# Performance work log

Hardware: AMD Instinct MI355X
Metric: run time of the kernel (lower is better)

## Reference

```python
import jax, jax.numpy as jnp
import numpy as np

B, S, DIM = 2, 2048, 2048
N_HEADS, N_KV_HEADS = 16, 4
HEAD_DIM = DIM // N_HEADS  # 128
N_REP = N_HEADS // N_KV_HEADS  # 4


def setup_inputs() -> dict:
    key = jax.random.key(0)
    ks = jax.random.split(key, 7)
    x = jax.random.normal(ks[0], (B, S, DIM), dtype=jnp.float32)
    cos = jax.random.uniform(ks[1], (S, HEAD_DIM // 2), dtype=jnp.float32)
    sin = jax.random.uniform(ks[2], (S, HEAD_DIM // 2), dtype=jnp.float32)
    sc = 1.0 / np.sqrt(DIM)
    wq = jax.random.normal(ks[3], (DIM, N_HEADS * HEAD_DIM), dtype=jnp.float32) * sc
    wk = jax.random.normal(ks[4], (DIM, N_KV_HEADS * HEAD_DIM), dtype=jnp.float32) * sc
    wv = jax.random.normal(ks[5], (DIM, N_KV_HEADS * HEAD_DIM), dtype=jnp.float32) * sc
    wo = jax.random.normal(ks[6], (N_HEADS * HEAD_DIM, DIM), dtype=jnp.float32) * sc
    return {"x": x, "cos": cos, "sin": sin, "wq": wq, "wk": wk, "wv": wv, "wo": wo}


def _rope(t, cos, sin):
    # t: [B, S, H, hd]; cos/sin: [S, hd/2] -> broadcast as [1, S, 1, hd/2]
    tr, ti = t[..., ::2], t[..., 1::2]
    c = cos[None, :, None, :]
    s = sin[None, :, None, :]
    out_r = tr * c - ti * s
    out_i = tr * s + ti * c
    # interleave back: stack on new last axis then flatten
    return jnp.stack([out_r, out_i], axis=-1).reshape(t.shape)


def reference(x, cos, sin, wq, wk, wv, wo):
    bsz, seqlen, _ = x.shape
    xq = (x @ wq).reshape(bsz, seqlen, N_HEADS, HEAD_DIM)
    xk = (x @ wk).reshape(bsz, seqlen, N_KV_HEADS, HEAD_DIM)
    xv = (x @ wv).reshape(bsz, seqlen, N_KV_HEADS, HEAD_DIM)
    xq = _rope(xq, cos, sin)
    xk = _rope(xk, cos, sin)
    # GQA: repeat kv heads -> [B, S, H, hd]
    xk = jnp.repeat(xk, N_REP, axis=2)
    xv = jnp.repeat(xv, N_REP, axis=2)
    scale = 1.0 / jnp.sqrt(jnp.asarray(HEAD_DIM, dtype=x.dtype))
    scores = jnp.einsum("bqhd,bkhd->bhqk", xq, xk) * scale
    causal = jnp.tril(jnp.ones((seqlen, seqlen), dtype=bool))
    scores = jnp.where(causal[None, None, :, :], scores, jnp.asarray(-jnp.inf, dtype=scores.dtype))
    attn = jax.nn.softmax(scores, axis=-1)
    out = jnp.einsum("bhqk,bkhd->bqhd", attn, xv)
    out = out.reshape(bsz, seqlen, N_HEADS * HEAD_DIM)
    return out @ wo
```

## Files before the change

kernel.cpp:

```cpp
#include <hip/hip_runtime.h>
#include <stdint.h>

#define SEQ 2048

typedef uint16_t u16;
typedef uint32_t u32;
typedef __attribute__((ext_vector_type(4))) float f32x4;
typedef __attribute__((ext_vector_type(8))) __bf16 bf16x8;

__device__ __forceinline__ u16 f2bf(float f) {
    u32 u = __float_as_uint(f);
    u += 0x7FFFu + ((u >> 16) & 1u);
    return (u16)(u >> 16);
}
__device__ __forceinline__ float bf2f(u16 h) {
    return __uint_as_float(((u32)h) << 16);
}
__device__ __forceinline__ void async16(const void* g, void* l) {
    auto gp = (__attribute__((address_space(1))) void*)const_cast<void*>(g);
    auto lp = (__attribute__((address_space(3))) void*)l;
    __builtin_amdgcn_global_load_lds(gp, lp, 16, 0, 0);
}

__global__ __launch_bounds__(256) void convert_bf16(const float* __restrict__ src,
                                                    u16* __restrict__ dst) {
    int i = blockIdx.x * 256 + threadIdx.x;
    float4 v = ((const float4*)src)[i];
    u32 lo = (u32)f2bf(v.x) | ((u32)f2bf(v.y) << 16);
    u32 hi = (u32)f2bf(v.z) | ((u32)f2bf(v.w) << 16);
    ((uint2*)dst)[i] = make_uint2(lo, hi);
}

__global__ __launch_bounds__(256) void tconv(const float* __restrict__ src,
                                             u16* __restrict__ dst, int N, int K) {
    __shared__ float tile[64][65];
    const int n0 = blockIdx.x * 64, k0 = blockIdx.y * 64;
    const int tid = threadIdx.x;
#pragma unroll
    for (int p = 0; p < 4; p++) {
        int r = p * 16 + (tid >> 4);
        int c = (tid & 15) * 4;
        float4 v = *(const float4*)&src[(size_t)(k0 + r) * N + n0 + c];
        tile[r][c] = v.x; tile[r][c+1] = v.y; tile[r][c+2] = v.z; tile[r][c+3] = v.w;
    }
    __syncthreads();
#pragma unroll
    for (int p = 0; p < 4; p++) {
        int n = p * 16 + (tid >> 4);
        int kq = (tid & 15) * 4;
        u32 lo = (u32)f2bf(tile[kq+0][n]) | ((u32)f2bf(tile[kq+1][n]) << 16);
        u32 hi = (u32)f2bf(tile[kq+2][n]) | ((u32)f2bf(tile[kq+3][n]) << 16);
        *(uint2*)&dst[(size_t)(n0 + n) * K + k0 + kq] = make_uint2(lo, hi);
    }
}

template <bool F32OUT>
__global__ __launch_bounds__(256) void gemm128(const u16* __restrict__ A,
                                               const u16* __restrict__ Bt,
                                               void* __restrict__ Cv,
                                               int M, int N, int K) {
    __shared__ u16 lA[128 * 32];
    __shared__ u16 lB[128 * 32];
    const int tid = threadIdx.x;
    const int m0 = blockIdx.y * 128, n0 = blockIdx.x * 128;
    const int lane = tid & 63;
    const int lr = lane & 15, quad = lane >> 4;
    const int w = tid >> 6;
    const int wm = (w >> 1) * 64, wn = (w & 1) * 64;

    f32x4 acc[4][4] = {};

    const int srow = tid >> 2;
    const int schunk = (tid & 3) ^ (srow & 3);
    const u16* aS0 = A  + (size_t)(m0 + srow) * K + schunk * 8;
    const u16* aS1 = aS0 + (size_t)64 * K;
    const u16* bS0 = Bt + (size_t)(n0 + srow) * K + schunk * 8;
    const u16* bS1 = bS0 + (size_t)64 * K;
    u16* lAd = lA + tid * 8;
    u16* lBd = lB + tid * 8;

    for (int k0 = 0; k0 < K; k0 += 32) {
        __syncthreads();
        async16(aS0 + k0, lAd);
        async16(aS1 + k0, lAd + 2048);
        async16(bS0 + k0, lBd);
        async16(bS1 + k0, lBd + 2048);
        __syncthreads();
        bf16x8 af[4], bfr[4];
        const int cs = (quad ^ (lr & 3)) * 8;
#pragma unroll
        for (int i = 0; i < 4; i++)
            af[i] = *(const bf16x8*)&lA[(wm + i * 16 + lr) * 32 + cs];
#pragma unroll
        for (int i = 0; i < 4; i++)
            bfr[i] = *(const bf16x8*)&lB[(wn + i * 16 + lr) * 32 + cs];
#pragma unroll
        for (int mf = 0; mf < 4; mf++)
#pragma unroll
            for (int nf = 0; nf < 4; nf++)
                acc[mf][nf] = __builtin_amdgcn_mfma_f32_16x16x32_bf16(
                    af[mf], bfr[nf], acc[mf][nf], 0, 0, 0);
    }

#pragma unroll
    for (int mf = 0; mf < 4; mf++) {
#pragma unroll
        for (int nf = 0; nf < 4; nf++) {
#pragma unroll
            for (int r = 0; r < 4; r++) {
                size_t row = (size_t)(m0 + wm + mf * 16 + quad * 4 + r);
                size_t col = (size_t)(n0 + wn + nf * 16 + lr);
                if (F32OUT)
                    ((float*)Cv)[row * (size_t)N + col] = acc[mf][nf][r];
                else
                    ((u16*)Cv)[row * (size_t)N + col] = f2bf(acc[mf][nf][r]);
            }
        }
    }
}

__global__ __launch_bounds__(256) void rope_qk(u16* __restrict__ qkv,
                                               const float* __restrict__ cosp,
                                               const float* __restrict__ sinp) {
    const int t = blockIdx.x;
    const int spos = t & (SEQ - 1);
    const int tid = threadIdx.x;
    const float qscale = 0.088388347762f * 1.4426950408889634f;
    u16* row = qkv + (size_t)t * 3072;
#pragma unroll
    for (int it = 0; it < 5; it++) {
        int p = it * 256 + tid;
        int col, ci; float sc2;
        if (p < 1024) { col = 2 * p; ci = p & 63; sc2 = qscale; }
        else          { int p2 = p - 1024; col = 2048 + 2 * p2; ci = p2 & 63; sc2 = 1.0f; }
        u32 v = *(u32*)(row + col);
        float tr = bf2f((u16)(v & 0xFFFFu));
        float ti = bf2f((u16)(v >> 16));
        float cs = cosp[spos * 64 + ci];
        float sn = sinp[spos * 64 + ci];
        float orr = (tr * cs - ti * sn) * sc2;
        float oi  = (tr * sn + ti * cs) * sc2;
        *(u32*)(row + col) = (u32)f2bf(orr) | ((u32)f2bf(oi) << 16);
    }
}

__global__ __launch_bounds__(256) void transpose_v(const u16* __restrict__ qkv,
                                                   u16* __restrict__ vt) {
    __shared__ u16 tile[64][65];
    const int bid = blockIdx.x;
    const int dt = bid & 1;
    const int st = (bid >> 1) & 31;
    const int kh = (bid >> 6) & 3;
    const int b  = bid >> 8;
    const int tid = threadIdx.x;
#pragma unroll
    for (int pp = 0; pp < 2; pp++) {
        int r  = pp * 32 + (tid >> 3);
        int c8 = (tid & 7) * 8;
        const u16* src = qkv + (size_t)(b * SEQ + st * 64 + r) * 3072 + 2560 + kh * 128 + dt * 64 + c8;
        uint4 v = *(const uint4*)src;
        tile[r][c8+0] = (u16)(v.x & 0xFFFF); tile[r][c8+1] = (u16)(v.x >> 16);
        tile[r][c8+2] = (u16)(v.y & 0xFFFF); tile[r][c8+3] = (u16)(v.y >> 16);
        tile[r][c8+4] = (u16)(v.z & 0xFFFF); tile[r][c8+5] = (u16)(v.z >> 16);
        tile[r][c8+6] = (u16)(v.w & 0xFFFF); tile[r][c8+7] = (u16)(v.w >> 16);
    }
    __syncthreads();
#pragma unroll
    for (int pp = 0; pp < 2; pp++) {
        int dr = pp * 32 + (tid >> 3);
        int s8 = (tid & 7) * 8;
        uint4 o;
        o.x = (u32)tile[s8+0][dr] | ((u32)tile[s8+1][dr] << 16);
        o.y = (u32)tile[s8+2][dr] | ((u32)tile[s8+3][dr] << 16);
        o.z = (u32)tile[s8+4][dr] | ((u32)tile[s8+5][dr] << 16);
        o.w = (u32)tile[s8+6][dr] | ((u32)tile[s8+7][dr] << 16);
        u16* dst = vt + ((size_t)((b * 4 + kh) * 128 + dt * 64 + dr)) * SEQ + st * 64 + s8;
        *(uint4*)dst = o;
    }
}

__global__ __launch_bounds__(256) void flash_attn(const u16* __restrict__ qkv,
                                                  const u16* __restrict__ vt,
                                                  u16* __restrict__ ob) {
    __shared__ u16 lK[2][64 * 128];
    __shared__ u16 lV[2][128 * 64];
    __shared__ u16 lP[4 * 16 * 64];
    const int bidx = blockIdx.x;
    const int qa = bidx & 15;
    const int h  = (bidx >> 4) & 15;
    const int b  = bidx >> 8;
    const int kh = h >> 2;
    const int tid = threadIdx.x;
    const int w = tid >> 6, lane = tid & 63;
    const int lr = lane & 15, quad = lane >> 4;

    const int krow = tid >> 4;
    const int kchunk = (tid & 15) ^ krow;
    const int vrow = tid >> 3;
    const int vchunk = (tid & 7) ^ (vrow & 7);
    const u16* kRow = qkv + (size_t)b * SEQ * 3072 + 2048 + kh * 128
                    + (size_t)krow * 3072 + kchunk * 8;
    const u16* vRow = vt + (size_t)(b * 4 + kh) * 128 * SEQ
                    + (size_t)vrow * SEQ + vchunk * 8;

    for (int half = 0; half < 2; half++) {
        const int qt = half ? qa : (31 - qa);

        bf16x8 qf[4];
        {
            const u16* qbase = qkv + (size_t)(b * SEQ + qt * 64 + w * 16 + lr) * 3072 + h * 128;
#pragma unroll
            for (int kk = 0; kk < 4; kk++)
                qf[kk] = *(const bf16x8*)(qbase + kk * 32 + quad * 8);
        }

        f32x4 o[8] = {};
        float mrow[4] = {-1e30f, -1e30f, -1e30f, -1e30f};
        float lrow[4] = {0.f, 0.f, 0.f, 0.f};

        {
            u16* lKd = &lK[0][0] + tid * 8;
            u16* lVd = &lV[0][0] + tid * 8;
#pragma unroll
            for (int i = 0; i < 4; i++)
                async16(kRow + (size_t)(i * 16) * 3072, lKd + i * 2048);
#pragma unroll
            for (int i = 0; i < 4; i++)
                async16(vRow + (size_t)(i * 32) * SEQ, lVd + i * 2048);
        }

        int nb = 0;
        for (int kt = 0; kt <= qt; kt++) {
            if (kt < qt) {
                u16* lKd = &lK[nb ^ 1][0] + tid * 8;
                u16* lVd = &lV[nb ^ 1][0] + tid * 8;
#pragma unroll
                for (int i = 0; i < 4; i++)
                    async16(kRow + (size_t)((kt + 1) * 64 + i * 16) * 3072, lKd + i * 2048);
#pragma unroll
                for (int i = 0; i < 4; i++)
                    async16(vRow + (size_t)(i * 32) * SEQ + (kt + 1) * 64, lVd + i * 2048);
                asm volatile("s_waitcnt vmcnt(8)" ::: "memory");
            } else {
                asm volatile("s_waitcnt vmcnt(0)" ::: "memory");
            }
            asm volatile("s_barrier" ::: "memory");

            const u16* lKc = &lK[nb][0];
            const u16* lVc = &lV[nb][0];

            f32x4 sc[4] = {};
#pragma unroll
            for (int nf = 0; nf < 4; nf++) {
#pragma unroll
                for (int kk = 0; kk < 4; kk++) {
                    bf16x8 bk = *(const bf16x8*)&lKc[(nf * 16 + lr) * 128 + (((kk * 4 + quad) ^ lr) * 8)];
                    sc[nf] = __builtin_amdgcn_mfma_f32_16x16x32_bf16(qf[kk], bk, sc[nf], 0, 0, 0);
                }
            }

            float sv[4][4];
            float mnew[4] = {mrow[0], mrow[1], mrow[2], mrow[3]};
            const bool diag = (kt == qt);
#pragma unroll
            for (int nf = 0; nf < 4; nf++)
#pragma unroll
                for (int r = 0; r < 4; r++) {
                    float v = sc[nf][r];
                    if (diag && (nf * 16 + lr) > (w * 16 + quad * 4 + r)) v = -1e30f;
                    sv[nf][r] = v;
                    mnew[r] = fmaxf(mnew[r], v);
                }
#pragma unroll
            for (int r = 0; r < 4; r++) {
                mnew[r] = fmaxf(mnew[r], __shfl_xor(mnew[r], 1, 16));
                mnew[r] = fmaxf(mnew[r], __shfl_xor(mnew[r], 2, 16));
                mnew[r] = fmaxf(mnew[r], __shfl_xor(mnew[r], 4, 16));
                mnew[r] = fmaxf(mnew[r], __shfl_xor(mnew[r], 8, 16));
            }
            float rsum[4] = {0.f, 0.f, 0.f, 0.f};
#pragma unroll
            for (int nf = 0; nf < 4; nf++)
#pragma unroll
                for (int r = 0; r < 4; r++) {
                    float e = exp2f(sv[nf][r] - mnew[r]);
                    sv[nf][r] = e;
                    rsum[r] += e;
                }
#pragma unroll
            for (int r = 0; r < 4; r++) {
                rsum[r] += __shfl_xor(rsum[r], 1, 16);
                rsum[r] += __shfl_xor(rsum[r], 2, 16);
                rsum[r] += __shfl_xor(rsum[r], 4, 16);
                rsum[r] += __shfl_xor(rsum[r], 8, 16);
            }
#pragma unroll
            for (int r = 0; r < 4; r++) {
                float alpha = exp2f(mrow[r] - mnew[r]);
                lrow[r] = lrow[r] * alpha + rsum[r];
                mrow[r] = mnew[r];
#pragma unroll
                for (int f = 0; f < 8; f++) o[f][r] *= alpha;
            }

#pragma unroll
            for (int nf = 0; nf < 4; nf++)
#pragma unroll
                for (int r = 0; r < 4; r++) {
                    int m_ = quad * 4 + r;
                    int khi = nf * 2 + (lr >> 3);
                    lP[w * 1024 + m_ * 64 + ((khi ^ (m_ & 7)) * 8) + (lr & 7)] = f2bf(sv[nf][r]);
                }

#pragma unroll
            for (int kf = 0; kf < 2; kf++) {
                bf16x8 pa = *(const bf16x8*)&lP[w * 1024 + lr * 64 + (((kf * 4 + quad) ^ (lr & 7)) * 8)];
#pragma unroll
                for (int nf = 0; nf < 8; nf++) {
                    bf16x8 vb = *(const bf16x8*)&lVc[(nf * 16 + lr) * 64 + (((kf * 4 + quad) ^ (lr & 7)) * 8)];
                    o[nf] = __builtin_amdgcn_mfma_f32_16x16x32_bf16(pa, vb, o[nf], 0, 0, 0);
                }
            }

            asm volatile("s_barrier" ::: "memory");
            nb ^= 1;
        }

        u16* obase = ob + (size_t)(b * SEQ + qt * 64 + w * 16) * 2048 + h * 128;
#pragma unroll
        for (int r = 0; r < 4; r++) {
            float rinv = 1.0f / lrow[r];
#pragma unroll
            for (int f = 0; f < 8; f++)
                obase[(quad * 4 + r) * 2048 + f * 16 + lr] = f2bf(o[f][r] * rinv);
        }
    }
}

extern "C" void kernel_launch(void* const* d_in, const int* in_sizes, int n_in,
                              void* d_out, int out_size, void* d_ws, size_t ws_size,
                              hipStream_t stream) {
    (void)in_sizes; (void)n_in; (void)out_size; (void)ws_size;
    const float* x    = (const float*)d_in[0];
    const float* cosp = (const float*)d_in[1];
    const float* sinp = (const float*)d_in[2];
    const float* wq   = (const float*)d_in[3];
    const float* wk   = (const float*)d_in[4];
    const float* wv   = (const float*)d_in[5];
    const float* wo   = (const float*)d_in[6];
    float* out = (float*)d_out;

    char* ws = (char*)d_ws;
    u16* xb    = (u16*)(ws);
    u16* qkvb  = (u16*)(ws + (size_t)16 * 1024 * 1024);
    u16* wqkvT = (u16*)(ws + (size_t)40 * 1024 * 1024);
    u16* woT   = (u16*)(ws + (size_t)52 * 1024 * 1024);
    u16* vtb   = (u16*)(ws + (size_t)60 * 1024 * 1024);
    u16* ob    = xb;

    convert_bf16<<<8192, 256, 0, stream>>>(x, xb);
    tconv<<<dim3(32, 32), 256, 0, stream>>>(wq, wqkvT, 2048, 2048);
    tconv<<<dim3( 8, 32), 256, 0, stream>>>(wk, wqkvT + (size_t)2048 * 2048, 512, 2048);
    tconv<<<dim3( 8, 32), 256, 0, stream>>>(wv, wqkvT + (size_t)2560 * 2048, 512, 2048);
    tconv<<<dim3(32, 32), 256, 0, stream>>>(wo, woT, 2048, 2048);
    gemm128<false><<<dim3(24, 32), 256, 0, stream>>>(xb, wqkvT, (void*)qkvb, 4096, 3072, 2048);
    rope_qk<<<4096, 256, 0, stream>>>(qkvb, cosp, sinp);
    transpose_v<<<512, 256, 0, stream>>>(qkvb, vtb);
    flash_attn<<<512, 256, 0, stream>>>(qkvb, vtb, ob);
    gemm128<true><<<dim3(16, 32), 256, 0, stream>>>(ob, woT, (void*)out, 4096, 2048, 2048);
}
```

Measured before the change: 363.0 us.

## Use 128-row query tiles with transposed S=K·Q^T MFMA and per-lane row softmax

The flash attention kernel now gives each block a 128-query tile, with each wave holding 32 query rows, so every K/V tile loaded into LDS feeds twice as many MFMAs. It replaces the paired-half scheme with a heavy-first block ordering. Scores are computed as K·Q^T, so each lane owns one query row, which reduces the softmax reductions to two cross-quad shuffles. P is written to LDS as packed 4-element stores. The cost is higher register pressure from doubled accumulators under launch_bounds(256,2), plus fewer, larger blocks with coarser load balance.

```diff
diff --git a/kernel.cpp b/kernel.cpp
--- a/kernel.cpp
+++ b/kernel.cpp
@@ -7,6 +7,7 @@
 typedef uint32_t u32;
 typedef __attribute__((ext_vector_type(4))) float f32x4;
 typedef __attribute__((ext_vector_type(8))) __bf16 bf16x8;
+typedef __attribute__((ext_vector_type(4))) __bf16 bf16x4;
 
 __device__ __forceinline__ u16 f2bf(float f) {
     u32 u = __float_as_uint(f);
@@ -179,20 +180,29 @@
     }
 }
 
-__global__ __launch_bounds__(256) void flash_attn(const u16* __restrict__ qkv,
-                                                  const u16* __restrict__ vt,
-                                                  u16* __restrict__ ob) {
+__global__ __launch_bounds__(256, 2) void flash_attn(const u16* __restrict__ qkv,
+                                                     const u16* __restrict__ vt,
+                                                     u16* __restrict__ ob) {
     __shared__ u16 lK[2][64 * 128];
     __shared__ u16 lV[2][128 * 64];
-    __shared__ u16 lP[4 * 16 * 64];
+    __shared__ u16 lP[4][32 * 64];
     const int bidx = blockIdx.x;
-    const int qa = bidx & 15;
-    const int h  = (bidx >> 4) & 15;
-    const int b  = bidx >> 8;
-    const int kh = h >> 2;
+    int bh, qt;
+    if (bidx < 256) { bh = bidx >> 3;         qt = 8 + (bidx & 7); }
+    else            { bh = (bidx - 256) >> 3; qt = 7 - ((bidx - 256) & 7); }
+    const int b = bh >> 4, h = bh & 15, kh = h >> 2;
     const int tid = threadIdx.x;
     const int w = tid >> 6, lane = tid & 63;
     const int lr = lane & 15, quad = lane >> 4;
+
+    bf16x8 qf[2][4];
+#pragma unroll
+    for (int qi = 0; qi < 2; qi++) {
+        const u16* qbase = qkv + (size_t)(b * SEQ + qt * 128 + w * 32 + qi * 16 + lr) * 3072 + h * 128;
+#pragma unroll
+        for (int kk = 0; kk < 4; kk++)
+            qf[qi][kk] = *(const bf16x8*)(qbase + kk * 32 + quad * 8);
+    }
 
     const int krow = tid >> 4;
     const int kchunk = (tid & 15) ^ krow;
@@ -203,136 +213,133 @@
     const u16* vRow = vt + (size_t)(b * 4 + kh) * 128 * SEQ
                     + (size_t)vrow * SEQ + vchunk * 8;
 
-    for (int half = 0; half < 2; half++) {
-        const int qt = half ? qa : (31 - qa);
-
-        bf16x8 qf[4];
-        {
-            const u16* qbase = qkv + (size_t)(b * SEQ + qt * 64 + w * 16 + lr) * 3072 + h * 128;
-#pragma unroll
-            for (int kk = 0; kk < 4; kk++)
-                qf[kk] = *(const bf16x8*)(qbase + kk * 32 + quad * 8);
-        }
-
-        f32x4 o[8] = {};
-        float mrow[4] = {-1e30f, -1e30f, -1e30f, -1e30f};
-        float lrow[4] = {0.f, 0.f, 0.f, 0.f};
-
-        {
-            u16* lKd = &lK[0][0] + tid * 8;
-            u16* lVd = &lV[0][0] + tid * 8;
+    f32x4 o[2][8] = {};
+    float m_st[2] = {-1e30f, -1e30f};
+    float l_st[2] = {0.f, 0.f};
+
+    const int nkt = 2 * qt + 2;
+    {
+        u16* lKd = &lK[0][0] + tid * 8;
+        u16* lVd = &lV[0][0] + tid * 8;
+#pragma unroll
+        for (int i = 0; i < 4; i++) async16(kRow + (size_t)(i * 16) * 3072, lKd + i * 2048);
+#pragma unroll
+        for (int i = 0; i < 4; i++) async16(vRow + (size_t)(i * 32) * SEQ, lVd + i * 2048);
+    }
+    const int qg = qt * 128 + w * 32 + lr;
+
+    int nb = 0;
+    for (int kt = 0; kt < nkt; kt++) {
+        if (kt + 1 < nkt) {
+            u16* lKd = &lK[nb ^ 1][0] + tid * 8;
+            u16* lVd = &lV[nb ^ 1][0] + tid * 8;
 #pragma unroll
             for (int i = 0; i < 4; i++)
-                async16(kRow + (size_t)(i * 16) * 3072, lKd + i * 2048);
+                async16(kRow + (size_t)((kt + 1) * 64 + i * 16) * 3072, lKd + i * 2048);
 #pragma unroll
             for (int i = 0; i < 4; i++)
-                async16(vRow + (size_t)(i * 32) * SEQ, lVd + i * 2048);
-        }
-
-        int nb = 0;
-        for (int kt = 0; kt <= qt; kt++) {
-            if (kt < qt) {
-                u16* lKd = &lK[nb ^ 1][0] + tid * 8;
-                u16* lVd = &lV[nb ^ 1][0] + tid * 8;
-#pragma unroll
-                for (int i = 0; i < 4; i++)
-                    async16(kRow + (size_t)((kt + 1) * 64 + i * 16) * 3072, lKd + i * 2048);
-#pragma unroll
-                for (int i = 0; i < 4; i++)
-                    async16(vRow + (size_t)(i * 32) * SEQ + (kt + 1) * 64, lVd + i * 2048);
-                asm volatile("s_waitcnt vmcnt(8)" ::: "memory");
-            } else {
-                asm volatile("s_waitcnt vmcnt(0)" ::: "memory");
-            }
-            asm volatile("s_barrier" ::: "memory");
-
-            const u16* lKc = &lK[nb][0];
-            const u16* lVc = &lV[nb][0];
-
-            f32x4 sc[4] = {};
+                async16(vRow + (size_t)(i * 32) * SEQ + (kt + 1) * 64, lVd + i * 2048);
+            asm volatile("s_waitcnt vmcnt(8)" ::: "memory");
+        } else {
+            asm volatile("s_waitcnt vmcnt(0)" ::: "memory");
+        }
+        asm volatile("s_barrier" ::: "memory");
+
+        const u16* lKc = &lK[nb][0];
+        const u16* lVc = &lV[nb][0];
+
+        f32x4 sc[2][4] = {};
+#pragma unroll
+        for (int nf = 0; nf < 4; nf++) {
+#pragma unroll
+            for (int kk = 0; kk < 4; kk++) {
+                bf16x8 ak = *(const bf16x8*)&lKc[(nf * 16 + lr) * 128 + (((kk * 4 + quad) ^ lr) * 8)];
+                sc[0][nf] = __builtin_amdgcn_mfma_f32_16x16x32_bf16(ak, qf[0][kk], sc[0][nf], 0, 0, 0);
+                sc[1][nf] = __builtin_amdgcn_mfma_f32_16x16x32_bf16(ak, qf[1][kk], sc[1][nf], 0, 0, 0);
+            }
+        }
+
+        const bool diag = (kt >= 2 * qt);
+        const int kb = kt * 64 + quad * 4;
+#pragma unroll
+        for (int qi = 0; qi < 2; qi++) {
+            float ps[4][4];
+            float mnew = m_st[qi];
+            const int qrow_g = qg + qi * 16;
+#pragma unroll
+            for (int nf = 0; nf < 4; nf++)
+#pragma unroll
+                for (int r = 0; r < 4; r++) {
+                    float v = sc[qi][nf][r];
+                    if (diag && (kb + nf * 16 + r) > qrow_g) v = -1e30f;
+                    ps[nf][r] = v;
+                    mnew = fmaxf(mnew, v);
+                }
+            mnew = fmaxf(mnew, __shfl_xor(mnew, 16));
+            mnew = fmaxf(mnew, __shfl_xor(mnew, 32));
+            float rsum = 0.f;
+#pragma unroll
+            for (int nf = 0; nf < 4; nf++)
+#pragma unroll
+                for (int r = 0; r < 4; r++) {
+                    float e = exp2f(ps[nf][r] - mnew);
+                    ps[nf][r] = e;
+                    rsum += e;
+                }
+            rsum += __shfl_xor(rsum, 16);
+            rsum += __shfl_xor(rsum, 32);
+            float alpha = exp2f(m_st[qi] - mnew);
+            l_st[qi] = l_st[qi] * alpha + rsum;
+            m_st[qi] = mnew;
+#pragma unroll
+            for (int r = 0; r < 4; r++) {
+                float ar = __shfl(alpha, quad * 4 + r, 16);
+#pragma unroll
+                for (int nd = 0; nd < 8; nd++) o[qi][nd][r] *= ar;
+            }
+            const int qrow = qi * 16 + lr;
 #pragma unroll
             for (int nf = 0; nf < 4; nf++) {
-#pragma unroll
-                for (int kk = 0; kk < 4; kk++) {
-                    bf16x8 bk = *(const bf16x8*)&lKc[(nf * 16 + lr) * 128 + (((kk * 4 + quad) ^ lr) * 8)];
-                    sc[nf] = __builtin_amdgcn_mfma_f32_16x16x32_bf16(qf[kk], bk, sc[nf], 0, 0, 0);
-                }
-            }
-
-            float sv[4][4];
-            float mnew[4] = {mrow[0], mrow[1], mrow[2], mrow[3]};
-            const bool diag = (kt == qt);
-#pragma unroll
-            for (int nf = 0; nf < 4; nf++)
-#pragma unroll
-                for (int r = 0; r < 4; r++) {
-                    float v = sc[nf][r];
-                    if (diag && (nf * 16 + lr) > (w * 16 + quad * 4 + r)) v = -1e30f;
-                    sv[nf][r] = v;
-                    mnew[r] = fmaxf(mnew[r], v);
-                }
-#pragma unroll
-            for (int r = 0; r < 4; r++) {
-                mnew[r] = fmaxf(mnew[r], __shfl_xor(mnew[r], 1, 16));
-                mnew[r] = fmaxf(mnew[r], __shfl_xor(mnew[r], 2, 16));
-                mnew[r] = fmaxf(mnew[r], __shfl_xor(mnew[r], 4, 16));
-                mnew[r] = fmaxf(mnew[r], __shfl_xor(mnew[r], 8, 16));
-            }
-            float rsum[4] = {0.f, 0.f, 0.f, 0.f};
-#pragma unroll
-            for (int nf = 0; nf < 4; nf++)
-#pragma unroll
-                for (int r = 0; r < 4; r++) {
-                    float e = exp2f(sv[nf][r] - mnew[r]);
-                    sv[nf][r] = e;
-                    rsum[r] += e;
-                }
-#pragma unroll
-            for (int r = 0; r < 4; r++) {
-                rsum[r] += __shfl_xor(rsum[r], 1, 16);
-                rsum[r] += __shfl_xor(rsum[r], 2, 16);
-                rsum[r] += __shfl_xor(rsum[r], 4, 16);
-                rsum[r] += __shfl_xor(rsum[r], 8, 16);
-            }
-#pragma unroll
-            for (int r = 0; r < 4; r++) {
-                float alpha = exp2f(mrow[r] - mnew[r]);
-                lrow[r] = lrow[r] * alpha + rsum[r];
-                mrow[r] = mnew[r];
-#pragma unroll
-                for (int f = 0; f < 8; f++) o[f][r] *= alpha;
-            }
-
-#pragma unroll
-            for (int nf = 0; nf < 4; nf++)
-#pragma unroll
-                for (int r = 0; r < 4; r++) {
-                    int m_ = quad * 4 + r;
-                    int khi = nf * 2 + (lr >> 3);
-                    lP[w * 1024 + m_ * 64 + ((khi ^ (m_ & 7)) * 8) + (lr & 7)] = f2bf(sv[nf][r]);
-                }
-
-#pragma unroll
-            for (int kf = 0; kf < 2; kf++) {
-                bf16x8 pa = *(const bf16x8*)&lP[w * 1024 + lr * 64 + (((kf * 4 + quad) ^ (lr & 7)) * 8)];
-#pragma unroll
-                for (int nf = 0; nf < 8; nf++) {
-                    bf16x8 vb = *(const bf16x8*)&lVc[(nf * 16 + lr) * 64 + (((kf * 4 + quad) ^ (lr & 7)) * 8)];
-                    o[nf] = __builtin_amdgcn_mfma_f32_16x16x32_bf16(pa, vb, o[nf], 0, 0, 0);
-                }
-            }
-
-            asm volatile("s_barrier" ::: "memory");
-            nb ^= 1;
-        }
-
-        u16* obase = ob + (size_t)(b * SEQ + qt * 64 + w * 16) * 2048 + h * 128;
+                u32 lo = (u32)f2bf(ps[nf][0]) | ((u32)f2bf(ps[nf][1]) << 16);
+                u32 hi = (u32)f2bf(ps[nf][2]) | ((u32)f2bf(ps[nf][3]) << 16);
+                int c = (nf * 4 + quad) ^ lr;
+                *(uint2*)&lP[w][qrow * 64 + c * 4] = make_uint2(lo, hi);
+            }
+        }
+
+#pragma unroll
+        for (int kf = 0; kf < 2; kf++) {
+            bf16x8 pa[2];
+#pragma unroll
+            for (int qi = 0; qi < 2; qi++) {
+                int c0 = (kf * 8 + quad * 2) ^ lr;
+                int c1 = (kf * 8 + quad * 2 + 1) ^ lr;
+                bf16x4 p0 = *(const bf16x4*)&lP[w][(qi * 16 + lr) * 64 + c0 * 4];
+                bf16x4 p1 = *(const bf16x4*)&lP[w][(qi * 16 + lr) * 64 + c1 * 4];
+                pa[qi] = __builtin_shufflevector(p0, p1, 0, 1, 2, 3, 4, 5, 6, 7);
+            }
+#pragma unroll
+            for (int nd = 0; nd < 8; nd++) {
+                bf16x8 vb = *(const bf16x8*)&lVc[(nd * 16 + lr) * 64 + (((kf * 4 + quad) ^ (lr & 7)) * 8)];
+                o[0][nd] = __builtin_amdgcn_mfma_f32_16x16x32_bf16(pa[0], vb, o[0][nd], 0, 0, 0);
+                o[1][nd] = __builtin_amdgcn_mfma_f32_16x16x32_bf16(pa[1], vb, o[1][nd], 0, 0, 0);
+            }
+        }
+
+        asm volatile("s_barrier" ::: "memory");
+        nb ^= 1;
+    }
+
+#pragma unroll
+    for (int qi = 0; qi < 2; qi++) {
+        float rinv = 1.0f / l_st[qi];
+        u16* obase = ob + (size_t)(b * SEQ + qt * 128 + w * 32 + qi * 16) * 2048 + h * 128;
 #pragma unroll
         for (int r = 0; r < 4; r++) {
-            float rinv = 1.0f / lrow[r];
-#pragma unroll
-            for (int f = 0; f < 8; f++)
-                obase[(quad * 4 + r) * 2048 + f * 16 + lr] = f2bf(o[f][r] * rinv);
+            float rv = __shfl(rinv, quad * 4 + r, 16);
+#pragma unroll
+            for (int nd = 0; nd < 8; nd++)
+                obase[(quad * 4 + r) * 2048 + nd * 16 + lr] = f2bf(o[qi][nd][r] * rv);
         }
     }
 }
```

Result: faster. 351.6 us (-3.1%).
